# Performance work log

Hardware: AMD Instinct MI355X
Metric: run time of the kernel (lower is better)

The kernel has to match this reference:

```python
import jax, jax.numpy as jnp
import numpy as np

D_MODEL = 1024
NUM_HEADS = 16
HEAD_DIM = D_MODEL // NUM_HEADS


def setup_inputs() -> dict:
    key = jax.random.key(0)
    k1, k2, k3 = jax.random.split(key, 3)
    B, S = 4, 2048
    x = jax.random.normal(k1, (B, S, D_MODEL), dtype=jnp.float32)
    # Linear weights; scale like torch's default-ish init for numerical sanity.
    w_qkv = jax.random.normal(k2, (D_MODEL, 3 * D_MODEL), dtype=jnp.float32) / np.sqrt(D_MODEL)
    b_qkv = jnp.zeros((3 * D_MODEL,), dtype=jnp.float32)
    w_out = jax.random.normal(k3, (D_MODEL, D_MODEL), dtype=jnp.float32) / np.sqrt(D_MODEL)
    b_out = jnp.zeros((D_MODEL,), dtype=jnp.float32)
    return {"x": x, "w_qkv": w_qkv, "b_qkv": b_qkv, "w_out": w_out, "b_out": b_out}


def reference(x, w_qkv, b_qkv, w_out, b_out):
    B, S, D = x.shape
    H, Hd = NUM_HEADS, HEAD_DIM
    # fused QKV projection, then chunk along last dim (same as torch.chunk)
    qkv = x @ w_qkv + b_qkv                       # [B, S, 3D]
    q, k, v = jnp.split(qkv, 3, axis=-1)          # each [B, S, D]
    q = q.reshape(B, S, H, Hd).transpose(0, 2, 1, 3)  # [B, H, S, Hd]
    k = k.reshape(B, S, H, Hd).transpose(0, 2, 1, 3)
    v = v.reshape(B, S, H, Hd).transpose(0, 2, 1, 3)
    scale = 1.0 / np.sqrt(Hd).astype(np.float32)
    scores = jnp.einsum('bhqd,bhkd->bhqk', q, k) * scale  # [B, H, S, S]
    attn = jax.nn.softmax(scores, axis=-1)
    out = jnp.einsum('bhqk,bhkd->bhqd', attn, v)           # [B, H, S, Hd]
    out = out.transpose(0, 2, 1, 3).reshape(B, S, D)
    return out @ w_out + b_out
```

## Files before the change

kernel.cpp:

```cpp
#include <hip/hip_runtime.h>
#include <stdint.h>

typedef unsigned short u16;
typedef __attribute__((ext_vector_type(8))) short   short8;
typedef __attribute__((ext_vector_type(8))) u16     ushort8;
typedef __attribute__((ext_vector_type(4))) float   f32x4;
typedef __attribute__((ext_vector_type(16))) float  f32x16;
typedef __attribute__((ext_vector_type(4))) unsigned int u32x4;

#define SEQ   2048
#define NH    16
#define HD    64
#define DM    1024
#define ROWS  8192
#define BHN   64

__device__ __forceinline__ u16 f2bf(float f){
  union { float f; uint32_t u; } v; v.f = f;
  return (u16)((v.u + 0x7fffu + ((v.u >> 16) & 1u)) >> 16);
}

__device__ __forceinline__ unsigned cvtpk(float a, float b){
  unsigned r;
  asm("v_cvt_pk_bf16_f32 %0, %1, %2" : "=v"(r) : "v"(a), "v"(b));
  return r;
}

__device__ __forceinline__ void pswap(unsigned &a, unsigned &b){
  asm volatile("v_permlane32_swap_b32 %0, %1" : "+v"(a), "+v"(b));
}

__device__ __forceinline__ float fexp2(float x){
  return __builtin_amdgcn_exp2f(x);
}

__device__ __forceinline__ float tsum16(const f32x16& s){
  float a0=s[0]+s[1], a1=s[2]+s[3], a2=s[4]+s[5], a3=s[6]+s[7];
  float a4=s[8]+s[9], a5=s[10]+s[11], a6=s[12]+s[13], a7=s[14]+s[15];
  float b0=a0+a1, b1=a2+a3, b2=a4+a5, b3=a6+a7;
  return (b0+b1)+(b2+b3);
}

#define GAS(p) ((const __attribute__((address_space(1))) void*)(p))
#define LAS(p) ((__attribute__((address_space(3))) void*)(p))

__global__ void prep_kernel(const float* __restrict__ x, u16* __restrict__ xb,
                            const float* __restrict__ wqkv, u16* __restrict__ wqkvT,
                            const float* __restrict__ wout, u16* __restrict__ woutT)
{
  __shared__ float tile[32][33];
  const int bid = blockIdx.x, tid = threadIdx.x;
  if (bid < 4096) {
    int i = bid * 256 + tid;
    const float4* p = (const float4*)x + (size_t)i * 2;
    float4 a = p[0], b = p[1];
    ushort8 o;
    o[0]=f2bf(a.x); o[1]=f2bf(a.y); o[2]=f2bf(a.z); o[3]=f2bf(a.w);
    o[4]=f2bf(b.x); o[5]=f2bf(b.y); o[6]=f2bf(b.z); o[7]=f2bf(b.w);
    *(ushort8*)(xb + (size_t)i * 8) = o;
    return;
  }
  const float* in; u16* out; int R, C, bx, by;
  if (bid < 7168) { in = wqkv; out = wqkvT; R = 1024; C = 3072; int b2 = bid - 4096; bx = b2 % 96; by = b2 / 96; }
  else            { in = wout; out = woutT; R = 1024; C = 1024; int b2 = bid - 7168; bx = b2 % 32; by = b2 / 32; }
  int c0 = bx * 32, r0 = by * 32;
  int tx = tid & 31, ty = tid >> 5;
  #pragma unroll
  for (int i = 0; i < 4; i++)
    tile[ty + 8*i][tx] = in[(size_t)(r0 + ty + 8*i) * C + c0 + tx];
  __syncthreads();
  #pragma unroll
  for (int i = 0; i < 4; i++)
    out[(size_t)(c0 + ty + 8*i) * R + r0 + tx] = f2bf(tile[tx][ty + 8*i]);
}

#define BM 128
#define BN 128
#define BK 64

template<int MODE>
__global__ __launch_bounds__(256, 2) void gemm_kernel(
    const u16* __restrict__ A, const u16* __restrict__ Bt, const float* __restrict__ bias,
    u16* __restrict__ Qo, u16* __restrict__ Ko, u16* __restrict__ Vto,
    float* __restrict__ Cout)
{
  __shared__ __align__(16) u16 As[BM * BK];
  __shared__ __align__(16) u16 Bs[BN * BK];
  const int tid  = threadIdx.x;
  const int lane = tid & 63, wv = tid >> 6;
  const int wr = wv >> 1, wc = wv & 1;
  const int m0 = blockIdx.y * BM, n0 = blockIdx.x * BN;
  const int K = 1024;

  f32x4 acc[4][4] = {};

  for (int k0 = 0; k0 < K; k0 += BK) {
    #pragma unroll
    for (int i = 0; i < 4; i++) {
      int f = (i * 256 + tid) * 16;
      int row = f >> 7, inrow = f & 127;
      int src = inrow ^ ((row & 7) << 4);
      const u16* ga = A  + (size_t)(m0 + row) * K + k0 + (src >> 1);
      __builtin_amdgcn_global_load_lds(GAS(ga), LAS((char*)As + (i*256 + (wv<<6))*16), 16, 0, 0);
      const u16* gb = Bt + (size_t)(n0 + row) * K + k0 + (src >> 1);
      __builtin_amdgcn_global_load_lds(GAS(gb), LAS((char*)Bs + (i*256 + (wv<<6))*16), 16, 0, 0);
    }
    __syncthreads();
    #pragma unroll
    for (int kk = 0; kk < 2; kk++) {
      short8 af[4], bfr[4];
      #pragma unroll
      for (int i = 0; i < 4; i++) {
        int row = wr*64 + i*16 + (lane & 15);
        int kb  = (kk*64 + 16*(lane >> 4)) ^ ((row & 7) << 4);
        af[i] = *(const short8*)((const char*)As + row*128 + kb);
      }
      #pragma unroll
      for (int j = 0; j < 4; j++) {
        int row = wc*64 + j*16 + (lane & 15);
        int kb  = (kk*64 + 16*(lane >> 4)) ^ ((row & 7) << 4);
        bfr[j] = *(const short8*)((const char*)Bs + row*128 + kb);
      }
      #pragma unroll
      for (int i = 0; i < 4; i++)
        #pragma unroll
        for (int j = 0; j < 4; j++)
          acc[i][j] = __builtin_amdgcn_mfma_f32_16x16x32_bf16(af[i], bfr[j], acc[i][j], 0, 0, 0);
    }
    __syncthreads();
  }

  if (MODE == 0) {
    const int part = n0 >> 10;
    #pragma unroll
    for (int i = 0; i < 4; i++) {
      int row = m0 + wr*64 + i*16 + ((lane >> 4) << 2);
      int b = row >> 11, s = row & 2047;
      #pragma unroll
      for (int j = 0; j < 4; j++) {
        int col = n0 + wc*64 + j*16 + (lane & 15);
        int cn = col & 1023, h = cn >> 6, d = cn & 63;
        int bh = b * NH + h;
        #pragma unroll
        for (int r = 0; r < 4; r++) {
          float v = acc[i][j][r] + bias[col];
          int ss = s + r;
          if (part == 0)      Qo [((size_t)bh*SEQ + ss)*HD + d] = f2bf(v * 0.18033688011f);
          else if (part == 1) Ko [((size_t)bh*SEQ + ss)*HD + d] = f2bf(v);
          else                Vto[((size_t)bh*HD  + d)*SEQ + ss] = f2bf(v);
        }
      }
    }
  } else {
    #pragma unroll
    for (int i = 0; i < 4; i++) {
      int row = m0 + wr*64 + i*16 + ((lane >> 4) << 2);
      #pragma unroll
      for (int j = 0; j < 4; j++) {
        int col = n0 + wc*64 + j*16 + (lane & 15);
        float bv = bias[col];
        #pragma unroll
        for (int r = 0; r < 4; r++)
          Cout[(size_t)(row + r) * DM + col] = acc[i][j][r] + bv;
      }
    }
  }
}

#define STAGE(LOFF, T) do { \
    _Pragma("unroll") \
    for (int _i = 0; _i < 2; _i++) { \
      int _row = _i * 32 + (tid >> 3); \
      int _src = (((tid & 7) << 4) ^ ((_row & 7) << 4)) >> 1; \
      const u16* _gk = Kg + (((size_t)bh * SEQ + (T) * 64 + _row) << 6) + _src; \
      __builtin_amdgcn_global_load_lds(GAS(_gk), LAS(lds + (LOFF) + _i * 4096 + (wv << 10)), 16, 0, 0); \
      const u16* _gv = Vt + ((size_t)(bh * 64 + _row)) * SEQ + (T) * 64 + _src; \
      __builtin_amdgcn_global_load_lds(GAS(_gv), LAS(lds + (LOFF) + 8192 + _i * 4096 + (wv << 10)), 16, 0, 0); \
    } \
  } while (0)

#define WAITBAR() do { \
    asm volatile("s_waitcnt vmcnt(0) lgkmcnt(0)\n\ts_barrier" ::: "memory"); \
  } while (0)

#define PACK_PA(S, PA0, PA1) do { \
    unsigned a0 = cvtpk((S)[0],  (S)[1]),  b0 = cvtpk((S)[4],  (S)[5]); \
    unsigned a1 = cvtpk((S)[2],  (S)[3]),  b1 = cvtpk((S)[6],  (S)[7]); \
    unsigned a2 = cvtpk((S)[8],  (S)[9]),  b2 = cvtpk((S)[12], (S)[13]); \
    unsigned a3 = cvtpk((S)[10], (S)[11]), b3 = cvtpk((S)[14], (S)[15]); \
    pswap(a0, b0); pswap(a1, b1); pswap(a2, b2); pswap(a3, b3); \
    (PA0).u = (u32x4){a0, a1, b0, b1}; \
    (PA1).u = (u32x4){a2, a3, b2, b3}; \
  } while (0)

#define TILE64(BOFF) do { \
    _Pragma("unroll") \
    for (int H = 0; H < 2; H++) { \
      short8 kf[4]; \
      _Pragma("unroll") \
      for (int kd = 0; kd < 4; kd++) \
        kf[kd] = *(const short8*)(lds + (BOFF) + (32*H + l31) * 128 + ((32*kd + 16*hi) ^ swz)); \
      f32x16 sA, sB; \
      _Pragma("unroll") for (int i = 0; i < 16; i++) { sA[i] = -16.f; sB[i] = -16.f; } \
      __builtin_amdgcn_s_setprio(1); \
      _Pragma("unroll") \
      for (int kd = 0; kd < 4; kd++) { \
        sA = __builtin_amdgcn_mfma_f32_32x32x16_bf16(kf[kd], qfA[kd], sA, 0, 0, 0); \
        sB = __builtin_amdgcn_mfma_f32_32x32x16_bf16(kf[kd], qfB[kd], sB, 0, 0, 0); \
      } \
      __builtin_amdgcn_s_setprio(0); \
      _Pragma("unroll") for (int i = 0; i < 16; i++) { sA[i] = fexp2(sA[i]); sB[i] = fexp2(sB[i]); } \
      lpA += tsum16(sA); lpB += tsum16(sB); \
      union { u32x4 u; short8 s8; } paA0, paA1, paB0, paB1; \
      PACK_PA(sA, paA0, paA1); \
      PACK_PA(sB, paB0, paB1); \
      __builtin_amdgcn_s_setprio(1); \
      _Pragma("unroll") \
      for (int ki = 0; ki < 2; ki++) { \
        int vo = (64*H + 32*ki + 16*hi) ^ swz; \
        short8 vb0 = *(const short8*)(lds + (BOFF) + 8192  + l31 * 128 + vo); \
        short8 vb1 = *(const short8*)(lds + (BOFF) + 12288 + l31 * 128 + vo); \
        const short8 pA = ki ? paA1.s8 : paA0.s8; \
        const short8 pB = ki ? paB1.s8 : paB0.s8; \
        oA0 = __builtin_amdgcn_mfma_f32_32x32x16_bf16(pA, vb0, oA0, 0, 0, 0); \
        oA1 = __builtin_amdgcn_mfma_f32_32x32x16_bf16(pA, vb1, oA1, 0, 0, 0); \
        oB0 = __builtin_amdgcn_mfma_f32_32x32x16_bf16(pB, vb0, oB0, 0, 0, 0); \
        oB1 = __builtin_amdgcn_mfma_f32_32x32x16_bf16(pB, vb1, oB1, 0, 0, 0); \
      } \
      __builtin_amdgcn_s_setprio(0); \
    } \
  } while (0)

__global__ __launch_bounds__(256, 2) void attn_kernel(
    const u16* __restrict__ Q, const u16* __restrict__ Kg,
    const u16* __restrict__ Vt, u16* __restrict__ O)
{
  __shared__ __align__(16) char lds[32768];
  const int tid = threadIdx.x, lane = tid & 63, wv = tid >> 6;
  const int l31 = lane & 31, hi = lane >> 5;
  const int swz = (lane & 7) << 4;

  int flat = blockIdx.x;
  int nid = (flat & 7) * 64 + (flat >> 3);
  int bh = nid >> 3;
  int q0 = (nid & 7) * 256;

  short8 qfA[4], qfB[4];
  {
    int qrow = q0 + wv * 64 + l31;
    const u16* qp = Q + (((size_t)bh * SEQ + qrow) << 6) + hi * 8;
    #pragma unroll
    for (int kd = 0; kd < 4; kd++) {
      qfA[kd] = *(const short8*)(qp + kd * 16);
      qfB[kd] = *(const short8*)(qp + 2048 + kd * 16);
    }
  }

  f32x16 oA0 = {}, oA1 = {}, oB0 = {}, oB1 = {};
  float lpA = 0.f, lpB = 0.f;

  STAGE(0, 0);
  WAITBAR();
  for (int t = 0; t < 32; t += 2) {
    STAGE(16384, t + 1);
    TILE64(0);
    WAITBAR();
    if (t + 2 < 32) STAGE(0, t + 2);
    TILE64(16384);
    WAITBAR();
  }

  float lfA = lpA + __shfl_xor(lpA, 32);
  float lfB = lpB + __shfl_xor(lpB, 32);
  int b = bh >> 4, h = bh & 15;
  int qbase = q0 + wv * 64;
  #pragma unroll
  for (int r = 0; r < 16; r++) {
    int qrow = (r & 3) + 8 * (r >> 2) + 4 * hi;
    float invA = 1.0f / __shfl(lfA, qrow);
    float invB = 1.0f / __shfl(lfB, qrow);
    size_t rowA = ((size_t)(b * SEQ + qbase + qrow) << 10) + h * 64 + l31;
    size_t rowB = rowA + (32u << 10);
    O[rowA]      = f2bf(oA0[r] * invA);
    O[rowA + 32] = f2bf(oA1[r] * invA);
    O[rowB]      = f2bf(oB0[r] * invB);
    O[rowB + 32] = f2bf(oB1[r] * invB);
  }
}

extern "C" void kernel_launch(void* const* d_in, const int* in_sizes, int n_in,
                              void* d_out, int out_size, void* d_ws, size_t ws_size,
                              hipStream_t stream)
{
  const float* x     = (const float*)d_in[0];
  const float* w_qkv = (const float*)d_in[1];
  const float* b_qkv = (const float*)d_in[2];
  const float* w_out = (const float*)d_in[3];
  const float* b_out = (const float*)d_in[4];
  float* out = (float*)d_out;

  char* w = (char*)d_ws;
  u16* xb    = (u16*)(w);
  u16* wqkvT = (u16*)(w + 16777216);
  u16* woutT = (u16*)(w + 23068672);
  u16* Qw    = (u16*)(w + 25165824);
  u16* Kw    = (u16*)(w + 41943040);
  u16* Vtw   = (u16*)(w + 58720256);
  u16* Ow    = (u16*)(w + 75497472);

  prep_kernel<<<dim3(8192), dim3(256), 0, stream>>>(x, xb, w_qkv, wqkvT, w_out, woutT);
  gemm_kernel<0><<<dim3(24, 64), dim3(256), 0, stream>>>(xb, wqkvT, b_qkv, Qw, Kw, Vtw, nullptr);
  attn_kernel<<<dim3(512), dim3(256), 0, stream>>>(Qw, Kw, Vtw, Ow);
  gemm_kernel<1><<<dim3(8, 64), dim3(256), 0, stream>>>(Ow, woutT, b_out, nullptr, nullptr, nullptr, out);
}
```

Before: 187.4 us.

## Load K/V fragments directly from global memory instead of LDS staging

Removes the double-buffered LDS staging of K and V tiles, along with the per-tile waitcnt/barrier synchronisation. Each wave now reads its K and V MFMA operands straight from global memory, relying on L1/L2 to serve the reuse across the four waves of a block. This drops barrier stalls and LDS traffic, but it gives up explicit prefetch overlap and multiplies global/L2 read traffic by the number of waves sharing each tile.

```diff
diff --git a/kernel.cpp b/kernel.cpp
--- a/kernel.cpp
+++ b/kernel.cpp
@@ -167,22 +167,6 @@
   }
 }
 
-#define STAGE(LOFF, T) do { \
-    _Pragma("unroll") \
-    for (int _i = 0; _i < 2; _i++) { \
-      int _row = _i * 32 + (tid >> 3); \
-      int _src = (((tid & 7) << 4) ^ ((_row & 7) << 4)) >> 1; \
-      const u16* _gk = Kg + (((size_t)bh * SEQ + (T) * 64 + _row) << 6) + _src; \
-      __builtin_amdgcn_global_load_lds(GAS(_gk), LAS(lds + (LOFF) + _i * 4096 + (wv << 10)), 16, 0, 0); \
-      const u16* _gv = Vt + ((size_t)(bh * 64 + _row)) * SEQ + (T) * 64 + _src; \
-      __builtin_amdgcn_global_load_lds(GAS(_gv), LAS(lds + (LOFF) + 8192 + _i * 4096 + (wv << 10)), 16, 0, 0); \
-    } \
-  } while (0)
-
-#define WAITBAR() do { \
-    asm volatile("s_waitcnt vmcnt(0) lgkmcnt(0)\n\ts_barrier" ::: "memory"); \
-  } while (0)
-
 #define PACK_PA(S, PA0, PA1) do { \
     unsigned a0 = cvtpk((S)[0],  (S)[1]),  b0 = cvtpk((S)[4],  (S)[5]); \
     unsigned a1 = cvtpk((S)[2],  (S)[3]),  b1 = cvtpk((S)[6],  (S)[7]); \
@@ -193,52 +177,12 @@
     (PA1).u = (u32x4){a2, a3, b2, b3}; \
   } while (0)
 
-#define TILE64(BOFF) do { \
-    _Pragma("unroll") \
-    for (int H = 0; H < 2; H++) { \
-      short8 kf[4]; \
-      _Pragma("unroll") \
-      for (int kd = 0; kd < 4; kd++) \
-        kf[kd] = *(const short8*)(lds + (BOFF) + (32*H + l31) * 128 + ((32*kd + 16*hi) ^ swz)); \
-      f32x16 sA, sB; \
-      _Pragma("unroll") for (int i = 0; i < 16; i++) { sA[i] = -16.f; sB[i] = -16.f; } \
-      __builtin_amdgcn_s_setprio(1); \
-      _Pragma("unroll") \
-      for (int kd = 0; kd < 4; kd++) { \
-        sA = __builtin_amdgcn_mfma_f32_32x32x16_bf16(kf[kd], qfA[kd], sA, 0, 0, 0); \
-        sB = __builtin_amdgcn_mfma_f32_32x32x16_bf16(kf[kd], qfB[kd], sB, 0, 0, 0); \
-      } \
-      __builtin_amdgcn_s_setprio(0); \
-      _Pragma("unroll") for (int i = 0; i < 16; i++) { sA[i] = fexp2(sA[i]); sB[i] = fexp2(sB[i]); } \
-      lpA += tsum16(sA); lpB += tsum16(sB); \
-      union { u32x4 u; short8 s8; } paA0, paA1, paB0, paB1; \
-      PACK_PA(sA, paA0, paA1); \
-      PACK_PA(sB, paB0, paB1); \
-      __builtin_amdgcn_s_setprio(1); \
-      _Pragma("unroll") \
-      for (int ki = 0; ki < 2; ki++) { \
-        int vo = (64*H + 32*ki + 16*hi) ^ swz; \
-        short8 vb0 = *(const short8*)(lds + (BOFF) + 8192  + l31 * 128 + vo); \
-        short8 vb1 = *(const short8*)(lds + (BOFF) + 12288 + l31 * 128 + vo); \
-        const short8 pA = ki ? paA1.s8 : paA0.s8; \
-        const short8 pB = ki ? paB1.s8 : paB0.s8; \
-        oA0 = __builtin_amdgcn_mfma_f32_32x32x16_bf16(pA, vb0, oA0, 0, 0, 0); \
-        oA1 = __builtin_amdgcn_mfma_f32_32x32x16_bf16(pA, vb1, oA1, 0, 0, 0); \
-        oB0 = __builtin_amdgcn_mfma_f32_32x32x16_bf16(pB, vb0, oB0, 0, 0, 0); \
-        oB1 = __builtin_amdgcn_mfma_f32_32x32x16_bf16(pB, vb1, oB1, 0, 0, 0); \
-      } \
-      __builtin_amdgcn_s_setprio(0); \
-    } \
-  } while (0)
-
 __global__ __launch_bounds__(256, 2) void attn_kernel(
     const u16* __restrict__ Q, const u16* __restrict__ Kg,
     const u16* __restrict__ Vt, u16* __restrict__ O)
 {
-  __shared__ __align__(16) char lds[32768];
   const int tid = threadIdx.x, lane = tid & 63, wv = tid >> 6;
   const int l31 = lane & 31, hi = lane >> 5;
-  const int swz = (lane & 7) << 4;
 
   int flat = blockIdx.x;
   int nid = (flat & 7) * 64 + (flat >> 3);
@@ -256,18 +200,54 @@
     }
   }
 
+  const u16* kp = Kg + (((size_t)bh * SEQ) << 6) + ((32*0 + l31) << 6) + 8*hi;
+  const u16* vp0 = Vt + ((size_t)(bh * 64 + l31)) * SEQ + 8*hi;
+  const u16* vp1 = Vt + ((size_t)(bh * 64 + 32 + l31)) * SEQ + 8*hi;
+
   f32x16 oA0 = {}, oA1 = {}, oB0 = {}, oB1 = {};
   float lpA = 0.f, lpB = 0.f;
 
-  STAGE(0, 0);
-  WAITBAR();
-  for (int t = 0; t < 32; t += 2) {
-    STAGE(16384, t + 1);
-    TILE64(0);
-    WAITBAR();
-    if (t + 2 < 32) STAGE(0, t + 2);
-    TILE64(16384);
-    WAITBAR();
+  for (int t = 0; t < 32; ++t) {
+    const int kb = t * 64;
+    #pragma unroll
+    for (int H = 0; H < 2; H++) {
+      const u16* kr = kp + (((size_t)(kb + 32*H)) << 6);
+      short8 kf[4];
+      #pragma unroll
+      for (int kd = 0; kd < 4; kd++)
+        kf[kd] = *(const short8*)(kr + kd * 16);
+
+      f32x16 sA, sB;
+      #pragma unroll
+      for (int i = 0; i < 16; i++) { sA[i] = -16.f; sB[i] = -16.f; }
+      __builtin_amdgcn_s_setprio(1);
+      #pragma unroll
+      for (int kd = 0; kd < 4; kd++) {
+        sA = __builtin_amdgcn_mfma_f32_32x32x16_bf16(kf[kd], qfA[kd], sA, 0, 0, 0);
+        sB = __builtin_amdgcn_mfma_f32_32x32x16_bf16(kf[kd], qfB[kd], sB, 0, 0, 0);
+      }
+      __builtin_amdgcn_s_setprio(0);
+      #pragma unroll
+      for (int i = 0; i < 16; i++) { sA[i] = fexp2(sA[i]); sB[i] = fexp2(sB[i]); }
+      lpA += tsum16(sA); lpB += tsum16(sB);
+      union { u32x4 u; short8 s8; } paA0, paA1, paB0, paB1;
+      PACK_PA(sA, paA0, paA1);
+      PACK_PA(sB, paB0, paB1);
+      __builtin_amdgcn_s_setprio(1);
+      #pragma unroll
+      for (int ki = 0; ki < 2; ki++) {
+        int ke = kb + 32*H + 16*ki;
+        short8 vb0 = *(const short8*)(vp0 + ke);
+        short8 vb1 = *(const short8*)(vp1 + ke);
+        const short8 pA = ki ? paA1.s8 : paA0.s8;
+        const short8 pB = ki ? paB1.s8 : paB0.s8;
+        oA0 = __builtin_amdgcn_mfma_f32_32x32x16_bf16(pA, vb0, oA0, 0, 0, 0);
+        oA1 = __builtin_amdgcn_mfma_f32_32x32x16_bf16(pA, vb1, oA1, 0, 0, 0);
+        oB0 = __builtin_amdgcn_mfma_f32_32x32x16_bf16(pB, vb0, oB0, 0, 0, 0);
+        oB1 = __builtin_amdgcn_mfma_f32_32x32x16_bf16(pB, vb1, oB1, 0, 0, 0);
+      }
+      __builtin_amdgcn_s_setprio(0);
+    }
   }
 
   float lfA = lpA + __shfl_xor(lpA, 32);
```

New measurement: 237.2 us. 26.6% more time.
